# Performance work log

Measured on AMD Instinct MI355X. Metric: run time of the kernel, lower is better.

The kernel has to match this reference:

```python
import jax, jax.numpy as jnp
import numpy as np

# ---- fixed physiological constants (match init_kwargs cell/synapse params) ----
DT = 0.1  # ms
N_CELL_TYPES = 2
S_REC, S_FF, S_TOT = 3, 1, 4
TAU_MEM = jnp.array([20.0, 10.0])
THETA = jnp.array([-50.0, -50.0])
U_RESET = jnp.array([-65.0, -65.0])
E_L = jnp.array([-70.0, -70.0])
G_L = jnp.array([10.0, 10.0])
TAU_REF_STEPS = jnp.round(jnp.array([2.0, 1.0]) / DT)  # [20, 10] steps
# combined recurrent(3) + FF(1) synapse channels
TAU_RISE = jnp.array([0.5, 2.0, 0.5, 0.5])
TAU_DECAY = jnp.array([2.0, 100.0, 5.0, 2.0])
E_SYN = jnp.array([0.0, 0.0, -80.0, 0.0])
G_BAR = jnp.array([1.0, 0.5, 1.0, 1.0])
SYN2CELL = jnp.array([0, 0, 1])  # recurrent synapse -> presynaptic cell type
A_RISE = jnp.exp(-DT / TAU_RISE)
A_DECAY = jnp.exp(-DT / TAU_DECAY)


def spike(x):
    return (x > 0).astype(x.dtype)


def setup_inputs() -> dict:
    key = jax.random.key(0)
    ks = jax.random.split(key, 8)
    N, NI, B, T = 4096, 1024, 8, 500
    ci = jax.random.randint(ks[0], (N,), 0, 2).astype(jnp.int32)  # 0=exc, 1=inh
    ci_ff = jnp.zeros((NI,), dtype=jnp.int32)
    # sparse signed recurrent weights (Dale's law: sign by presynaptic type)
    mag = jnp.abs(jax.random.normal(ks[1], (N, N))) * 0.02
    sign = jnp.where(ci == 1, -1.0, 1.0)[:, None]
    mask = jax.random.bernoulli(ks[2], 0.1, (N, N))
    weights = (mag * sign * mask).astype(jnp.float32)
    # sparse positive feedforward weights
    mag_ff = jnp.abs(jax.random.normal(ks[3], (NI, N))) * 0.05
    mask_ff = jax.random.bernoulli(ks[4], 0.2, (NI, N))
    weights_FF = (mag_ff * mask_ff).astype(jnp.float32)
    scaling_factors = jax.random.uniform(ks[5], (2, 2), minval=0.5, maxval=1.5)
    scaling_factors_FF = jax.random.uniform(ks[6], (1, 2), minval=0.5, maxval=1.5)
    input_spikes = (jax.random.uniform(ks[7], (B, T, NI)) < 0.05).astype(jnp.float32)
    return {
        "input_spikes": input_spikes,
        "weights": weights,
        "weights_FF": weights_FF,
        "scaling_factors": scaling_factors,
        "scaling_factors_FF": scaling_factors_FF,
        "cell_type_indices": ci,
        "cell_type_indices_FF": ci_ff,
    }


def reference(input_spikes, weights, weights_FF, scaling_factors, scaling_factors_FF,
              cell_type_indices, cell_type_indices_FF):
    ci = cell_type_indices
    B, T, NI = input_spikes.shape
    N = weights.shape[0]
    # per-neuron parameter gathers
    tau_mem = TAU_MEM[ci]
    theta = THETA[ci]
    u_reset = U_RESET[ci]
    e_l = E_L[ci]
    g_l = G_L[ci]
    ref_steps = TAU_REF_STEPS[ci]
    # cell-type pairwise scaling applied to (masked) weights
    W_eff = weights * scaling_factors[ci[:, None], ci[None, :]]            # (N,N)
    Wff_eff = weights_FF * scaling_factors_FF[cell_type_indices_FF[:, None], ci[None, :]]
    cell_masks = jnp.stack([(ci == c).astype(weights.dtype) for c in range(N_CELL_TYPES)])  # (2,N)
    # precompute feedforward synaptic drive for all timesteps: (T,B,N)
    drive_ff = jnp.einsum('bti,ij->tbj', input_spikes, Wff_eff) * G_BAR[S_REC]

    v0 = jnp.broadcast_to(e_l, (B, N))
    h0 = jnp.zeros((B, N, S_TOT), weights.dtype)
    g0 = jnp.zeros((B, N, S_TOT), weights.dtype)
    ref0 = jnp.zeros((B, N), weights.dtype)
    s0 = jnp.zeros((B, N), weights.dtype)

    def step(carry, dff_t):
        v, h, g, ref, s_prev = carry
        # recurrent drive split by presynaptic cell type, routed to synapse channels
        drive_c = jnp.stack([(s_prev * cell_masks[c]) @ W_eff for c in range(N_CELL_TYPES)], axis=-1)  # (B,N,2)
        drive_rec = drive_c[..., SYN2CELL] * G_BAR[:S_REC]                  # (B,N,3)
        drive = jnp.concatenate([drive_rec, dff_t[..., None]], axis=-1)    # (B,N,4)
        # double-exponential conductance kinetics
        h = h * A_RISE + drive
        g = g * A_DECAY + (1.0 - A_DECAY) * h
        # conductance-based membrane update
        I_syn = jnp.sum(g * (E_SYN - v[..., None]), axis=-1)                # (B,N)
        v_new = v + (DT / tau_mem) * ((e_l - v) + I_syn / g_l)
        refr = (ref > 0).astype(v.dtype)
        v_new = refr * u_reset + (1.0 - refr) * v_new
        s_new = spike(v_new - theta) * (1.0 - refr)
        spk = s_new > 0.5
        v_post = jnp.where(spk, u_reset, v_new)
        ref_new = jnp.where(spk, ref_steps, jnp.maximum(ref - 1.0, 0.0))
        return (v_post, h, g, ref_new, s_new), s_new

    _, spikes = jax.lax.scan(step, (v0, h0, g0, ref0, s0), drive_ff)
    return jnp.transpose(spikes, (1, 0, 2))  # (B,T,N)
```

## Files before the change

kernel.cpp:

```cpp
#include <hip/hip_runtime.h>
#include <cstdint>
#include <cstddef>

#define N_NEU   4096
#define N_IN    1024
#define B_SZ    8
#define T_STEPS 500
#define NSLICE  16
#define NBLK    (B_SZ * NSLICE)
#define FF_WORDS (B_SZ * T_STEPS * 16)

#define WS_TM_OFF   0
#define WS_MB_OFF   512
#define WS_FFM_OFF  17408
#define WS_FFD_OFF  529408
#define WS_NEED_FFD (529408 + (size_t)T_STEPS * B_SZ * N_NEU * 4)

__global__ __launch_bounds__(64) void snn_init(const int* __restrict__ ci,
                                               unsigned long long* __restrict__ tmask,
                                               unsigned long long* __restrict__ mb2) {
    const int k = blockIdx.x, l = threadIdx.x;
    unsigned long long m = __ballot(ci[(k << 6) + l] == 0);
    if (l == 0) tmask[k] = m;
    const int idx = (k << 6) + l;
    if (idx < 2048) mb2[idx] = 0ULL;
}

__global__ __launch_bounds__(256) void snn_ffmask(const float* __restrict__ inspk,
                                                  unsigned long long* __restrict__ ffmask) {
    int gid = blockIdx.x * 256 + threadIdx.x;
    int wid = gid >> 6, lane = gid & 63;
    int nw  = (gridDim.x * 256) >> 6;
    for (int w = wid; w < FF_WORDS; w += nw) {
        float v = inspk[(size_t)w * 64 + lane];
        unsigned long long m = __ballot(v > 0.5f);
        if (lane == 0) ffmask[w] = m;
    }
}

__device__ __forceinline__ int extract_pad(unsigned long long m,
                                           unsigned long long tm_exc,
                                           int* lds, int lane) {
    int pc  = __popcll(m);
    int sum = pc;
#pragma unroll
    for (int d = 1; d < 64; d <<= 1) {
        int o = __shfl_up(sum, d, 64);
        if (lane >= d) sum += o;
    }
    int off   = sum - pc;
    int total = __shfl(sum, 63, 64);
    int base  = lane << 6;
    while (m) {
        int bit = __builtin_ctzll(m);
        int ty  = ((tm_exc >> bit) & 1ULL) ? 0 : 1;
        lds[off++] = ((base + bit) << 2) | ty;
        m &= m - 1ULL;
    }
    int padcnt = (-total) & 63;
    if (lane < padcnt) lds[total + lane] = 2;
    return total;
}

__device__ __forceinline__ void gather2(const int* __restrict__ lst, int npad,
                                        const float* __restrict__ base,
                                        float se, float si,
                                        float* oe, float* oi) {
#pragma clang fp contract(off)
    float ae = 0.0f, ai = 0.0f;
    const int4* lst4 = (const int4*)lst;
    for (int k = 0; k < npad; k += 64) {
        int4  eq[16];
        int   e[64];
        float w[64];
#pragma unroll
        for (int u = 0; u < 16; ++u) eq[u] = lst4[(k >> 2) + u];
#pragma unroll
        for (int u = 0; u < 16; ++u) {
            e[4 * u + 0] = eq[u].x; e[4 * u + 1] = eq[u].y;
            e[4 * u + 2] = eq[u].z; e[4 * u + 3] = eq[u].w;
        }
#pragma unroll
        for (int u = 0; u < 64; ++u) w[u] = base[(size_t)(e[u] >> 2) << 12];
#pragma unroll
        for (int u = 0; u < 64; ++u) {
            const int ty = e[u] & 3;
            const float sc = (ty == 0) ? se : ((ty == 1) ? si : 0.0f);
            const float p  = w[u] * sc;
            ae = (ty == 0) ? ae + p : ae;
            ai = (ty == 1) ? ai + p : ai;
        }
    }
    *oe = ae; *oi = ai;
}

__global__ __launch_bounds__(64) void snn_ffpre(const unsigned long long* __restrict__ ffmask,
                                                const float* __restrict__ Wff,
                                                const float* __restrict__ sfff,
                                                const int*   __restrict__ ci,
                                                float*       __restrict__ ffdrive) {
#pragma clang fp contract(off)
    const int lane  = threadIdx.x;
    const int chunk = blockIdx.x & 63;
    const int tile  = blockIdx.x >> 6;
    const int i     = (chunk << 6) + lane;
    const float s_ff = sfff[ci[i]];
    __shared__ alignas(16) int lds_f[N_IN + 64];
    for (int p = tile * 25; p < tile * 25 + 25; ++p) {
        const int t = p >> 3, b = p & 7;
        const unsigned long long mf =
            (lane < 16) ? ffmask[((size_t)b * T_STEPS + t) * 16 + lane] : 0ULL;
        const int n = extract_pad(mf, ~0ULL, lds_f, lane);
        float fd, dummy;
        gather2(lds_f, (n + 63) & ~63, Wff + i, s_ff, 0.0f, &fd, &dummy);
        ffdrive[((size_t)t * B_SZ + b) * N_NEU + i] = fd;
    }
}

__global__ __launch_bounds__(256) void snn_run(
    const float* __restrict__ W,
    const float* __restrict__ Wff,
    const float* __restrict__ sf,
    const float* __restrict__ sfff,
    const int*   __restrict__ ci,
    float*       __restrict__ out,
    const unsigned long long* __restrict__ ffmask,
    const unsigned long long* __restrict__ tmask_g,
    const float* __restrict__ ffdrive,
    int use_ffpre,
    unsigned long long* __restrict__ mb2)
{
#pragma clang fp contract(off)
    const int tid   = threadIdx.x;
    const int lane  = tid & 63;
    const int wv    = tid >> 6;
    const int bid   = blockIdx.x;
    const int slice = (((bid >> 6) & 1) << 3) | (bid & 7);
    const int b     = (bid >> 3) & 7;
    const int i     = (slice << 8) + (wv << 6) + lane;
    const int c     = ci[i];

    const float s_exc = sf[c];
    const float s_inh = sf[2 + c];
    const float s_ff  = sfff[c];

    const unsigned long long my_tm = tmask_g[lane];

    __shared__ alignas(16) int lds_c[4][N_NEU + 64];
    __shared__ alignas(16) int lds_f[4][N_IN + 64];
    int* const my_ldsc = lds_c[wv];
    int* const my_ldsf = lds_f[wv];

    unsigned long long* const mbB = mb2 + (size_t)b * 128;

    float v = -70.0f, rf = 0.0f;
    float h0 = 0.0f, h1 = 0.0f, h2 = 0.0f, h3 = 0.0f;
    float g0 = 0.0f, g1 = 0.0f, g2 = 0.0f, g3 = 0.0f;

    const float aR0 = expf(-0.1f / 0.5f);
    const float aR1 = expf(-0.1f / 2.0f);
    const float aD0 = expf(-0.1f / 2.0f);
    const float aD1 = expf(-0.1f / 100.0f);
    const float aD2 = expf(-0.1f / 5.0f);
    const float kmem   = c ? (0.1f / 10.0f) : (0.1f / 20.0f);
    const float rsteps = c ? 10.0f : 20.0f;

    const float* const wseg = W + (size_t)((slice << 8) + (wv << 6));

    for (int t = 0; t < T_STEPS; ++t) {
        float ffd = 0.0f;
        if (use_ffpre) {
            ffd = ffdrive[((size_t)t * B_SZ + b) * N_NEU + i];
            asm volatile("" :: "v"(ffd));
        }

        unsigned long long mw = 0ULL;
        if (t > 0) {
            const unsigned int tg = (unsigned int)t;
            const unsigned long long* ep =
                mbB + (size_t)(t & 1) * 1024 + ((size_t)lane << 1);
            unsigned long long w0, w1;
            for (;;) {
                w0 = __hip_atomic_load(&ep[0], __ATOMIC_RELAXED,
                                       __HIP_MEMORY_SCOPE_AGENT);
                w1 = __hip_atomic_load(&ep[1], __ATOMIC_RELAXED,
                                       __HIP_MEMORY_SCOPE_AGENT);
                const bool ok = ((unsigned int)(w0 >> 32) == tg) &&
                                ((unsigned int)(w1 >> 32) == tg);
                if (__ballot(ok) == ~0ULL) break;
                __builtin_amdgcn_s_sleep(1);
            }
            mw = (w0 & 0xFFFFFFFFULL) | ((w1 & 0xFFFFFFFFULL) << 32);
            asm volatile("" ::: "memory");
        }

        {
            unsigned long long mm = mw;
            float wacc = 0.0f;
            const size_t rowbase = (size_t)lane << 18;
            while (mm) {
                const int bit = __builtin_ctzll(mm); mm &= mm - 1ULL;
                const float* r = wseg + rowbase + ((size_t)bit << 12);
                wacc += r[0]; wacc += r[16]; wacc += r[32]; wacc += r[48];
            }
            asm volatile("" :: "v"(wacc));
        }

        int ne = 0;
        if (__ballot(mw != 0ULL) != 0ULL)
            ne = extract_pad(mw, my_tm, my_ldsc, lane);

        if (!use_ffpre) {
            const unsigned long long mf =
                (lane < 16) ? ffmask[((size_t)b * T_STEPS + t) * 16 + lane] : 0ULL;
            const int nf = extract_pad(mf, ~0ULL, my_ldsf, lane);
            float fd, dummy;
            gather2(my_ldsf, (nf + 63) & ~63, Wff + i, s_ff, 0.0f, &fd, &dummy);
            ffd = fd;
        }

        float exc, inh;
        gather2(my_ldsc, (ne + 63) & ~63, W + i, s_exc, s_inh, &exc, &inh);

        const float d0 = exc;
        const float d1 = 0.5f * exc;
        const float d2 = inh;
        const float d3 = ffd;

        h0 = fmaf(h0, aR0, d0);
        h1 = fmaf(h1, aR1, d1);
        h2 = fmaf(h2, aR0, d2);
        h3 = fmaf(h3, aR0, d3);
        g0 = fmaf(g0, aD0, (1.0f - aD0) * h0);
        g1 = fmaf(g1, aD1, (1.0f - aD1) * h1);
        g2 = fmaf(g2, aD2, (1.0f - aD2) * h2);
        g3 = fmaf(g3, aD0, (1.0f - aD0) * h3);

        const float p0 = g0 * (0.0f - v);
        const float p1 = g1 * (0.0f - v);
        const float p2 = g2 * (-80.0f - v);
        const float p3 = g3 * (0.0f - v);
        const float Isyn = ((p0 + p1) + p2) + p3;

        float vn = fmaf(kmem, (-70.0f - v) + Isyn / 10.0f, v);
        const bool refr = rf > 0.0f;
        if (refr) vn = -65.0f;
        const float sn = (!refr && (vn > -50.0f)) ? 1.0f : 0.0f;
        const bool spk = sn > 0.5f;

        const unsigned long long sm = __ballot(spk);
        if (lane == 0) {
            const unsigned long long tg =
                (unsigned long long)(unsigned int)(t + 1) << 32;
            unsigned long long* pp = mb2 + (size_t)((t + 1) & 1) * 1024
                                   + (size_t)b * 128
                                   + ((size_t)((slice << 2) | wv) << 1);
            __hip_atomic_store(&pp[0], tg | (sm & 0xFFFFFFFFULL),
                               __ATOMIC_RELAXED, __HIP_MEMORY_SCOPE_AGENT);
            __hip_atomic_store(&pp[1], tg | (sm >> 32),
                               __ATOMIC_RELAXED, __HIP_MEMORY_SCOPE_AGENT);
        }

        v  = spk ? -65.0f : vn;
        rf = spk ? rsteps : fmaxf(rf - 1.0f, 0.0f);
        out[((size_t)b * T_STEPS + t) * N_NEU + i] = sn;
    }
}

extern "C" void kernel_launch(void* const* d_in, const int* in_sizes, int n_in,
                              void* d_out, int out_size, void* d_ws, size_t ws_size,
                              hipStream_t stream) {
    const float* inspk = (const float*)d_in[0];
    const float* W     = (const float*)d_in[1];
    const float* Wff   = (const float*)d_in[2];
    const float* sf    = (const float*)d_in[3];
    const float* sfff  = (const float*)d_in[4];
    const int*   ci    = (const int*)d_in[5];

    float* out = (float*)d_out;
    unsigned long long* tmask   = (unsigned long long*)((char*)d_ws + WS_TM_OFF);
    unsigned long long* mb2     = (unsigned long long*)((char*)d_ws + WS_MB_OFF);
    unsigned long long* ffmask  = (unsigned long long*)((char*)d_ws + WS_FFM_OFF);
    float*              ffdrive = (float*)((char*)d_ws + WS_FFD_OFF);
    const int use_ffpre = (ws_size >= WS_NEED_FFD) ? 1 : 0;

    snn_init<<<64, 64, 0, stream>>>(ci, tmask, mb2);
    snn_ffmask<<<1000, 256, 0, stream>>>(inspk, ffmask);
    if (use_ffpre)
        snn_ffpre<<<160 * 64, 64, 0, stream>>>(ffmask, Wff, sfff, ci, ffdrive);
    snn_run<<<NBLK, 256, 0, stream>>>(W, Wff, sf, sfff, ci, out,
                                      ffmask, tmask, ffdrive, use_ffpre, mb2);
}
```

Measured before the change: 977.3 us.

## Replace FF precompute kernel with in-loop prefetched feedforward gather

Drops the separate snn_ffpre kernel and its large ffdrive workspace buffer. The feedforward weight loads for step t+1 are now issued at the end of step t inside snn_run, so they overlap with the inter-block spin-wait barrier, and are summed at the start of the next step. This removes an extra launch plus the write and read of ffdrive, at the cost of 64 extra registers for the prefetched weights, which may reduce occupancy or cause spills.

```diff
diff --git a/kernel.cpp b/kernel.cpp
--- a/kernel.cpp
+++ b/kernel.cpp
@@ -13,8 +13,6 @@
 #define WS_TM_OFF   0
 #define WS_MB_OFF   512
 #define WS_FFM_OFF  17408
-#define WS_FFD_OFF  529408
-#define WS_NEED_FFD (529408 + (size_t)T_STEPS * B_SZ * N_NEU * 4)
 
 __global__ __launch_bounds__(64) void snn_init(const int* __restrict__ ci,
                                                unsigned long long* __restrict__ tmask,
@@ -94,27 +92,32 @@
     *oe = ae; *oi = ai;
 }
 
-__global__ __launch_bounds__(64) void snn_ffpre(const unsigned long long* __restrict__ ffmask,
-                                                const float* __restrict__ Wff,
-                                                const float* __restrict__ sfff,
-                                                const int*   __restrict__ ci,
-                                                float*       __restrict__ ffdrive) {
+__device__ __forceinline__ void ff_issue(const int* __restrict__ lds,
+                                         const float* __restrict__ base,
+                                         float* wf) {
+    const int4* l4 = (const int4*)lds;
+    int4 eq[16];
+#pragma unroll
+    for (int u = 0; u < 16; ++u) eq[u] = l4[u];
+#pragma unroll
+    for (int u = 0; u < 16; ++u) {
+        wf[4 * u + 0] = base[(size_t)(eq[u].x >> 2) << 12];
+        wf[4 * u + 1] = base[(size_t)(eq[u].y >> 2) << 12];
+        wf[4 * u + 2] = base[(size_t)(eq[u].z >> 2) << 12];
+        wf[4 * u + 3] = base[(size_t)(eq[u].w >> 2) << 12];
+    }
+}
+
+__device__ __forceinline__ float ff_fold(const float* wf, int nf, float sff) {
 #pragma clang fp contract(off)
-    const int lane  = threadIdx.x;
-    const int chunk = blockIdx.x & 63;
-    const int tile  = blockIdx.x >> 6;
-    const int i     = (chunk << 6) + lane;
-    const float s_ff = sfff[ci[i]];
-    __shared__ alignas(16) int lds_f[N_IN + 64];
-    for (int p = tile * 25; p < tile * 25 + 25; ++p) {
-        const int t = p >> 3, b = p & 7;
-        const unsigned long long mf =
-            (lane < 16) ? ffmask[((size_t)b * T_STEPS + t) * 16 + lane] : 0ULL;
-        const int n = extract_pad(mf, ~0ULL, lds_f, lane);
-        float fd, dummy;
-        gather2(lds_f, (n + 63) & ~63, Wff + i, s_ff, 0.0f, &fd, &dummy);
-        ffdrive[((size_t)t * B_SZ + b) * N_NEU + i] = fd;
-    }
+    float af = 0.0f;
+#pragma unroll
+    for (int u = 0; u < 64; ++u) {
+        const float sc = (u < nf) ? sff : 0.0f;
+        const float p  = wf[u] * sc;
+        af += p;
+    }
+    return af;
 }
 
 __global__ __launch_bounds__(256) void snn_run(
@@ -126,8 +129,6 @@
     float*       __restrict__ out,
     const unsigned long long* __restrict__ ffmask,
     const unsigned long long* __restrict__ tmask_g,
-    const float* __restrict__ ffdrive,
-    int use_ffpre,
     unsigned long long* __restrict__ mb2)
 {
 #pragma clang fp contract(off)
@@ -166,14 +167,19 @@
     const float rsteps = c ? 10.0f : 20.0f;
 
     const float* const wseg = W + (size_t)((slice << 8) + (wv << 6));
+    const float* const wffb = Wff + i;
+
+    float wf[64];
+    int   nf = 0;
+
+    {
+        const unsigned long long mf =
+            (lane < 16) ? ffmask[(size_t)b * T_STEPS * 16 + lane] : 0ULL;
+        nf = extract_pad(mf, ~0ULL, my_ldsf, lane);
+        if (nf > 0) ff_issue(my_ldsf, wffb, wf);
+    }
 
     for (int t = 0; t < T_STEPS; ++t) {
-        float ffd = 0.0f;
-        if (use_ffpre) {
-            ffd = ffdrive[((size_t)t * B_SZ + b) * N_NEU + i];
-            asm volatile("" :: "v"(ffd));
-        }
-
         unsigned long long mw = 0ULL;
         if (t > 0) {
             const unsigned int tg = (unsigned int)t;
@@ -194,6 +200,24 @@
             asm volatile("" ::: "memory");
         }
 
+        float ffd = 0.0f;
+        if (nf > 0) {
+            ffd = ff_fold(wf, nf, s_ff);
+            if (nf > 64) {
+                const int npadf = (nf + 63) & ~63;
+                for (int k = 64; k < npadf; k += 64) {
+#pragma unroll
+                    for (int u = 0; u < 64; ++u) {
+                        const int e = my_ldsf[k + u];
+                        const float w = wffb[(size_t)(e >> 2) << 12];
+                        const float sc = ((e & 3) == 0) ? s_ff : 0.0f;
+                        const float p  = w * sc;
+                        ffd += p;
+                    }
+                }
+            }
+        }
+
         {
             unsigned long long mm = mw;
             float wacc = 0.0f;
@@ -209,15 +233,6 @@
         int ne = 0;
         if (__ballot(mw != 0ULL) != 0ULL)
             ne = extract_pad(mw, my_tm, my_ldsc, lane);
-
-        if (!use_ffpre) {
-            const unsigned long long mf =
-                (lane < 16) ? ffmask[((size_t)b * T_STEPS + t) * 16 + lane] : 0ULL;
-            const int nf = extract_pad(mf, ~0ULL, my_ldsf, lane);
-            float fd, dummy;
-            gather2(my_ldsf, (nf + 63) & ~63, Wff + i, s_ff, 0.0f, &fd, &dummy);
-            ffd = fd;
-        }
 
         float exc, inh;
         gather2(my_ldsc, (ne + 63) & ~63, W + i, s_exc, s_inh, &exc, &inh);
@@ -264,6 +279,14 @@
         v  = spk ? -65.0f : vn;
         rf = spk ? rsteps : fmaxf(rf - 1.0f, 0.0f);
         out[((size_t)b * T_STEPS + t) * N_NEU + i] = sn;
+
+        if (t + 1 < T_STEPS) {
+            const unsigned long long mf =
+                (lane < 16) ? ffmask[((size_t)b * T_STEPS + (t + 1)) * 16 + lane]
+                            : 0ULL;
+            nf = extract_pad(mf, ~0ULL, my_ldsf, lane);
+            if (nf > 0) ff_issue(my_ldsf, wffb, wf);
+        }
     }
 }
 
@@ -278,16 +301,12 @@
     const int*   ci    = (const int*)d_in[5];
 
     float* out = (float*)d_out;
-    unsigned long long* tmask   = (unsigned long long*)((char*)d_ws + WS_TM_OFF);
-    unsigned long long* mb2     = (unsigned long long*)((char*)d_ws + WS_MB_OFF);
-    unsigned long long* ffmask  = (unsigned long long*)((char*)d_ws + WS_FFM_OFF);
-    float*              ffdrive = (float*)((char*)d_ws + WS_FFD_OFF);
-    const int use_ffpre = (ws_size >= WS_NEED_FFD) ? 1 : 0;
+    unsigned long long* tmask  = (unsigned long long*)((char*)d_ws + WS_TM_OFF);
+    unsigned long long* mb2    = (unsigned long long*)((char*)d_ws + WS_MB_OFF);
+    unsigned long long* ffmask = (unsigned long long*)((char*)d_ws + WS_FFM_OFF);
 
     snn_init<<<64, 64, 0, stream>>>(ci, tmask, mb2);
     snn_ffmask<<<1000, 256, 0, stream>>>(inspk, ffmask);
-    if (use_ffpre)
-        snn_ffpre<<<160 * 64, 64, 0, stream>>>(ffmask, Wff, sfff, ci, ffdrive);
     snn_run<<<NBLK, 256, 0, stream>>>(W, Wff, sf, sfff, ci, out,
-                                      ffmask, tmask, ffdrive, use_ffpre, mb2);
-}
+                                      ffmask, tmask, mb2);
+}
```

After: 1.621 ms. 1.66x slower.

## Stage feedforward weight column slice in LDS and sum spikes per neuron

Applied to the files above, without the earlier changes.

Replaces the feedforward precompute kernel with one that loads a 1024x32 column slice of Wff into shared memory (padded stride 33) per block. Each half-wave then walks the spike bitmask of one (t,b) pair with ctz and accumulates LDS weights, so Wff is no longer re-gathered from global memory for every time/batch pair. The grid drops to 128 blocks of 512 threads with about 132KB of LDS each, which gives low occupancy. The data-dependent while loops may also diverge across lanes.

```diff
diff --git a/kernel.cpp b/kernel.cpp
--- a/kernel.cpp
+++ b/kernel.cpp
@@ -9,6 +9,7 @@
 #define NSLICE  16
 #define NBLK    (B_SZ * NSLICE)
 #define FF_WORDS (B_SZ * T_STEPS * 16)
+#define FFP_STRIDE 33
 
 #define WS_TM_OFF   0
 #define WS_MB_OFF   512
@@ -94,26 +95,53 @@
     *oe = ae; *oi = ai;
 }
 
-__global__ __launch_bounds__(64) void snn_ffpre(const unsigned long long* __restrict__ ffmask,
-                                                const float* __restrict__ Wff,
-                                                const float* __restrict__ sfff,
-                                                const int*   __restrict__ ci,
-                                                float*       __restrict__ ffdrive) {
+__global__ __launch_bounds__(512) void snn_ffpre2(
+    const unsigned long long* __restrict__ ffmask,
+    const float* __restrict__ Wff,
+    const float* __restrict__ sfff,
+    const int*   __restrict__ ci,
+    float*       __restrict__ ffdrive)
+{
 #pragma clang fp contract(off)
-    const int lane  = threadIdx.x;
-    const int chunk = blockIdx.x & 63;
-    const int tile  = blockIdx.x >> 6;
-    const int i     = (chunk << 6) + lane;
-    const float s_ff = sfff[ci[i]];
-    __shared__ alignas(16) int lds_f[N_IN + 64];
-    for (int p = tile * 25; p < tile * 25 + 25; ++p) {
-        const int t = p >> 3, b = p & 7;
-        const unsigned long long mf =
-            (lane < 16) ? ffmask[((size_t)b * T_STEPS + t) * 16 + lane] : 0ULL;
-        const int n = extract_pad(mf, ~0ULL, lds_f, lane);
-        float fd, dummy;
-        gather2(lds_f, (n + 63) & ~63, Wff + i, s_ff, 0.0f, &fd, &dummy);
-        ffdrive[((size_t)t * B_SZ + b) * N_NEU + i] = fd;
+    const int tid = threadIdx.x;
+    const int s   = blockIdx.x;
+    __shared__ float lwff[N_IN * FFP_STRIDE];
+
+    {
+        const int j  = tid & 31;
+        const int r0 = tid >> 5;
+        for (int r = r0; r < N_IN; r += 16)
+            lwff[r * FFP_STRIDE + j] = Wff[(size_t)r * N_NEU + (s << 5) + j];
+    }
+    __syncthreads();
+
+    const int lane = tid & 63;
+    const int wv   = tid >> 6;
+    const int j    = lane & 31;
+    const int half = lane >> 5;
+    const int jg   = (s << 5) + j;
+    const float sff = sfff[ci[jg]];
+
+    for (int k = 0; k < 250; ++k) {
+        const int tb = (((k << 3) | wv) << 1) | half;
+        const int t  = tb >> 3, b = tb & 7;
+        const unsigned long long* mp = ffmask + ((size_t)b * T_STEPS + t) * 16;
+        unsigned long long mws[16];
+#pragma unroll
+        for (int w16 = 0; w16 < 16; ++w16) mws[w16] = mp[w16];
+        float acc = 0.0f;
+#pragma unroll
+        for (int w16 = 0; w16 < 16; ++w16) {
+            unsigned long long mw = mws[w16];
+            const int base = w16 << 6;
+            while (mw) {
+                const int bit = __builtin_ctzll(mw); mw &= mw - 1ULL;
+                const float w = lwff[(base + bit) * FFP_STRIDE + j];
+                const float p = w * sff;
+                acc += p;
+            }
+        }
+        ffdrive[((size_t)t * B_SZ + b) * N_NEU + jg] = acc;
     }
 }
 
@@ -287,7 +315,7 @@
     snn_init<<<64, 64, 0, stream>>>(ci, tmask, mb2);
     snn_ffmask<<<1000, 256, 0, stream>>>(inspk, ffmask);
     if (use_ffpre)
-        snn_ffpre<<<160 * 64, 64, 0, stream>>>(ffmask, Wff, sfff, ci, ffdrive);
+        snn_ffpre2<<<128, 512, 0, stream>>>(ffmask, Wff, sfff, ci, ffdrive);
     snn_run<<<NBLK, 256, 0, stream>>>(W, Wff, sf, sfff, ci, out,
                                       ffmask, tmask, ffdrive, use_ffpre, mb2);
 }
```

New measurement: 1.716 ms. +75.6%, slower.
